# Kernel optimization log

Hardware: AMD Instinct MI355X
Metric: run time of the kernel (lower is better)

The kernel has to match this reference:

```python
import jax, jax.numpy as jnp
import numpy as np
import math

B, S, HID, H = 2, 2048, 1024, 16
D = HID // H  # head_dim = 64

def _get_slopes(n):
    # power-of-2 branch (n=16)
    start = 2 ** (-2 ** (-(math.log2(n) - 3)))
    return np.array([start * 2 ** (-i) for i in range(n)], dtype=np.float32)

def setup_inputs() -> dict:
    key = jax.random.key(0)
    ks = jax.random.split(key, 9)
    sc = 1.0 / math.sqrt(HID)
    return {
        "x":  jax.random.normal(ks[0], (B, S, HID), dtype=jnp.float32),
        "Wq": jax.random.normal(ks[1], (HID, HID), dtype=jnp.float32) * sc,
        "bq": jnp.zeros((HID,), dtype=jnp.float32),
        "Wk": jax.random.normal(ks[2], (HID, HID), dtype=jnp.float32) * sc,
        "bk": jnp.zeros((HID,), dtype=jnp.float32),
        "Wv": jax.random.normal(ks[3], (HID, HID), dtype=jnp.float32) * sc,
        "bv": jnp.zeros((HID,), dtype=jnp.float32),
        "Wo": jax.random.normal(ks[4], (HID, HID), dtype=jnp.float32) * sc,
        "bo": jnp.zeros((HID,), dtype=jnp.float32),
        "slopes": jnp.asarray(_get_slopes(H)),
    }

def reference(x, Wq, bq, Wk, bk, Wv, bv, Wo, bo, slopes):
    b, s, hid = x.shape
    h = slopes.shape[0]
    d = hid // h
    # projections (torch Linear: y = x @ W.T + b), split heads -> [b,h,s,d]
    q = (x @ Wq.T + bq).reshape(b, s, h, d).transpose(0, 2, 1, 3)
    k = (x @ Wk.T + bk).reshape(b, s, h, d).transpose(0, 2, 1, 3)
    v = (x @ Wv.T + bv).reshape(b, s, h, d).transpose(0, 2, 1, 3)
    scores = jnp.einsum('bhqd,bhkd->bhqk', q, k) / jnp.sqrt(jnp.float32(d))
    # ALiBi bias: slope_h * (j - i), shape [h,s,s]
    pos = jnp.arange(s)
    dist = (pos[None, :] - pos[:, None]).astype(x.dtype)  # [s,s]
    scores = scores + slopes[None, :, None, None] * dist[None, None]
    attn = jax.nn.softmax(scores, axis=-1)
    ctx = jnp.einsum('bhqk,bhkd->bhqd', attn, v)
    ctx = ctx.transpose(0, 2, 1, 3).reshape(b, s, hid)
    return ctx @ Wo.T + bo
```

## Files before the change

kernel.cpp:

```cpp
#include <hip/hip_runtime.h>
#include <stdint.h>

typedef __attribute__((ext_vector_type(8))) short bf16x8;
typedef __attribute__((ext_vector_type(4))) short bf16x4;
typedef __attribute__((ext_vector_type(4))) float f32x4;
typedef unsigned short u16t;

#define DEVINL static __device__ __forceinline__

DEVINL u16t f2bf(float f) {
  union { float f; unsigned u; } v; v.f = f;
  return (u16t)((v.u + 0x7FFFu + ((v.u >> 16) & 1u)) >> 16);
}
DEVINL float bf2f(u16t u) {
  union { unsigned u; float f; } v; v.u = ((unsigned)u) << 16; return v.f;
}

DEVINL float exp2_fast(float x) {
  float r; asm("v_exp_f32 %0, %1" : "=v"(r) : "v"(x)); return r;
}
DEVINL unsigned cvt_pk_bf16(float a, float b) {
  unsigned r; asm("v_cvt_pk_bf16_f32 %0, %1, %2" : "=v"(r) : "v"(a), "v"(b)); return r;
}
DEVINL float max3f(float a, float b, float c) {
  float r; asm("v_max3_f32 %0, %1, %2, %3" : "=v"(r) : "v"(a), "v"(b), "v"(c)); return r;
}

DEVINL void gload16(const void* g, void* l) {
  __builtin_amdgcn_global_load_lds((const __attribute__((address_space(1))) void*)g,
                                   (__attribute__((address_space(3))) void*)l, 16, 0, 0);
}

__global__ __launch_bounds__(256)
void cvt5_kernel(const float* __restrict__ x, const float* __restrict__ wq,
                 const float* __restrict__ wk, const float* __restrict__ wv,
                 const float* __restrict__ wo, u16t* __restrict__ x_bf,
                 u16t* __restrict__ wqkv, u16t* __restrict__ wo_bf) {
  const int bid = blockIdx.x;
  const float* src; u16t* dst; int off;
  if (bid < 2048) { src = x; dst = x_bf; off = bid * 2048; }
  else {
    const int j = bid - 2048, sel = j >> 9;
    off = (j & 511) * 2048;
    if (sel == 0)      { src = wq; dst = wqkv; }
    else if (sel == 1) { src = wk; dst = wqkv + 1048576; }
    else if (sel == 2) { src = wv; dst = wqkv + 2097152; }
    else               { src = wo; dst = wo_bf; }
  }
  const int i = off + threadIdx.x * 8;
  float4 a = *(const float4*)(src + i);
  float4 b = *(const float4*)(src + i + 4);
  union { bf16x8 v; u16t u[8]; } o;
  o.u[0] = f2bf(a.x); o.u[1] = f2bf(a.y); o.u[2] = f2bf(a.z); o.u[3] = f2bf(a.w);
  o.u[4] = f2bf(b.x); o.u[5] = f2bf(b.y); o.u[6] = f2bf(b.z); o.u[7] = f2bf(b.w);
  *(bf16x8*)(dst + i) = o.v;
}

template <int MODE>
__global__ __launch_bounds__(256, 3)
void gemm_kernel(const u16t* __restrict__ A, const u16t* __restrict__ Bw,
                 const float* __restrict__ bias0, const float* __restrict__ bias1,
                 const float* __restrict__ bias2, void* __restrict__ outp) {
  __shared__ __attribute__((aligned(16))) u16t As[128 * 64];
  __shared__ __attribute__((aligned(16))) u16t Bs[128 * 64];
  const int tid = threadIdx.x;
  const int w = tid >> 6, l = tid & 63;
  const int wm = w >> 1, wn = w & 1;
  const int bm = blockIdx.x, bn = blockIdx.y;
  const int g = l >> 4, r16 = l & 15;
  const int srow = l >> 3, sslot = l & 7;

  f32x4 acc[4][4];
#pragma unroll
  for (int m = 0; m < 4; ++m)
#pragma unroll
    for (int n = 0; n < 4; ++n) acc[m][n] = f32x4{0.f, 0.f, 0.f, 0.f};

  const size_t arow0 = (size_t)bm * 128;
  const size_t brow0 = (size_t)bn * 128;

  for (int kt = 0; kt < 16; ++kt) {
    __syncthreads();
#pragma unroll
    for (int i = 0; i < 4; ++i) {
      const int row = (i * 4 + w) * 8 + srow;
      const int colA = kt * 64 + ((sslot ^ (row & 7)) * 8);
      gload16(A + (arow0 + row) * 1024 + colA, (char*)As + (i * 4 + w) * 1024);
      gload16(Bw + (brow0 + row) * 1024 + colA, (char*)Bs + (i * 4 + w) * 1024);
    }
    asm volatile("s_waitcnt vmcnt(0)" ::: "memory");
    __syncthreads();
#pragma unroll
    for (int kk = 0; kk < 2; ++kk) {
      bf16x8 af[4], bfr[4];
#pragma unroll
      for (int m = 0; m < 4; ++m) {
        const int rr = wm * 64 + m * 16 + r16;
        af[m] = *(const bf16x8*)((const char*)As + rr * 128 + (((kk * 4 + g) ^ (rr & 7)) * 16));
      }
#pragma unroll
      for (int n = 0; n < 4; ++n) {
        const int rr = wn * 64 + n * 16 + r16;
        bfr[n] = *(const bf16x8*)((const char*)Bs + rr * 128 + (((kk * 4 + g) ^ (rr & 7)) * 16));
      }
#pragma unroll
      for (int m = 0; m < 4; ++m)
#pragma unroll
        for (int n = 0; n < 4; ++n)
          acc[m][n] = __builtin_amdgcn_mfma_f32_16x16x32_bf16(af[m], bfr[n], acc[m][n], 0, 0, 0);
    }
  }

  if (MODE == 0) {
    const int mat = bn >> 3;
    if (mat == 2) {
      u16t* vt = (u16t*)outp + 8388608u;
#pragma unroll
      for (int n = 0; n < 4; ++n) {
        const int col = ((bn & 7) * 128) + wn * 64 + n * 16 + r16;
        const int hh = col >> 6, dd = col & 63;
        const float bv = bias2[col];
#pragma unroll
        for (int m = 0; m < 4; ++m) {
          const int row0 = bm * 128 + wm * 64 + m * 16 + g * 4;
          const int b_ = row0 >> 11, s_ = row0 & 2047;
          union { bf16x4 v; u16t u[4]; } o4;
#pragma unroll
          for (int i = 0; i < 4; ++i) o4.u[i] = f2bf(acc[m][n][i] + bv);
          *(bf16x4*)(vt + ((size_t)(b_ * 16 + hh) * 64 + dd) * 2048 + s_) = o4.v;
        }
      }
    } else {
      const float* bias = (mat == 0) ? bias0 : bias1;
      const float scale = (mat == 0) ? 0.18033688f : 1.0f;
      u16t* o = (u16t*)outp + (size_t)mat * 4194304u;
#pragma unroll
      for (int n = 0; n < 4; ++n) {
        const int col = ((bn & 7) * 128) + wn * 64 + n * 16 + r16;
        const float bv = bias[col];
#pragma unroll
        for (int m = 0; m < 4; ++m) {
          const int row = bm * 128 + wm * 64 + m * 16 + g * 4;
#pragma unroll
          for (int i = 0; i < 4; ++i)
            o[(size_t)(row + i) * 1024 + col] = f2bf((acc[m][n][i] + bv) * scale);
        }
      }
    }
  } else {
    float* o = (float*)outp;
#pragma unroll
    for (int n = 0; n < 4; ++n) {
      const int col = bn * 128 + wn * 64 + n * 16 + r16;
      const float bv = bias0[col];
#pragma unroll
      for (int m = 0; m < 4; ++m) {
        const int row = bm * 128 + wm * 64 + m * 16 + g * 4;
#pragma unroll
        for (int i = 0; i < 4; ++i)
          o[(size_t)(row + i) * 1024 + col] = acc[m][n][i] + bv;
      }
    }
  }
}

__global__ __launch_bounds__(256, 2)
void attn_kernel(const u16t* __restrict__ Qb, const u16t* __restrict__ Kb,
                 const u16t* __restrict__ Vtb, const float* __restrict__ slopes,
                 u16t* __restrict__ O0, u16t* __restrict__ O1,
                 float2* __restrict__ ML) {
  __shared__ __attribute__((aligned(16))) u16t Kl[3][2048];
  __shared__ __attribute__((aligned(16))) u16t Vl[2][2048];
  const int tid = threadIdx.x;
  const int w = tid >> 6, l = tid & 63;
  const int g = l >> 4, r = l & 15;
  const int qt = blockIdx.x;
  const int slot = blockIdx.y >> 1, b = blockIdx.y & 1;
  int h, sp;
  if (slot < 10)       { h = 6 + slot;  sp = 1; }
  else if (slot < 19)  { h = slot - 3;  sp = 0; }
  else if (slot == 19) { h = 5; sp = 1; }
  else if (slot == 20) { h = 6; sp = 0; }
  else if (slot < 26)  { h = 25 - slot; sp = 1; }
  else                 { h = slot - 26; sp = 0; }
  const float slope2 = slopes[h] * 1.44269504f;
  const int qpos = qt * 64 + w * 16 + r;
  const size_t base = (size_t)b * 2097152 + (size_t)h * 64;

  const float Wkeys = 26.0f / slope2;
  const int wt = (int)ceilf(Wkeys * 0.03125f);
  const int n = sp ? (wt < 32 ? wt : 32)
                   : (wt - 32 < 0 ? 0 : (wt - 32 < 32 ? wt - 32 : 32));
  if (n == 0) {
    if (l < 16)
      ML[((size_t)(sp * 2 + b) * 16 + h) * 2048 + qpos] = float2{-3.0e38f, 0.f};
    return;
  }

  const u16t* qrow = Qb + base + (size_t)qpos * 1024;
  const bf16x8 qf0 = *(const bf16x8*)(qrow + g * 8);
  const bf16x8 qf1 = *(const bf16x8*)(qrow + 32 + g * 8);
  asm volatile("s_waitcnt vmcnt(0)" ::: "memory");

  const int sig = 8 * (r >> 2) + (r & 3);
  const int toffs[2] = {0, 4};
  int koff[2][2], voff[4];
#pragma unroll
  for (int t = 0; t < 2; ++t) {
    const int row = toffs[t] + sig;
    const int mk = (row & 3) ^ ((row >> 1) & 4);
#pragma unroll
    for (int hh = 0; hh < 2; ++hh) koff[t][hh] = row * 128 + (((hh * 4 + g) ^ mk) * 16);
  }
#pragma unroll
  for (int db = 0; db < 4; ++db)
    voff[db] = (8 * db + (r >> 1)) * 128 + ((((((r & 1) << 2) | g)) ^ ((r >> 1) & 3)) * 16);

  const int kline_s = w * 8 + (l >> 3);
  const int ku_s = ((l & 7) ^ ((kline_s & 3) ^ ((kline_s >> 1) & 4))) * 8;
  const int vu_s = (l & 7) ^ (kline_s & 3);
  const int vd_s = 2 * kline_s + (vu_s >> 2);
  const int vcol_s = (vu_s & 3) * 8;

  f32x4 cv[2];
#pragma unroll
  for (int t = 0; t < 2; ++t)
#pragma unroll
    for (int i = 0; i < 4; ++i) cv[t][i] = slope2 * (float)(toffs[t] + 8 * g + i);

  const float d32 = slope2 * 32.f;
  float mj = -3.0e38f;
  f32x4 oc[4], sacc;
#pragma unroll
  for (int d = 0; d < 4; ++d) oc[d] = f32x4{0.f, 0.f, 0.f, 0.f};
  sacc = f32x4{0.f, 0.f, 0.f, 0.f};
  union { bf16x8 v; u16t u[8]; } ones;
#pragma unroll
  for (int i = 0; i < 8; ++i) ones.u[i] = 0x3F80;

  const u16t* Krow = Kb + base;
  const u16t* Vrow = Vtb + (size_t)(b * 16 + h) * 131072;
  const int kt0 = sp * 32 + 31;

#define STAGE_K(kt_, b_)                                                          \
  gload16(Krow + (size_t)((kt_) * 32 + kline_s) * 1024 + ku_s,                    \
          (char*)Kl + (b_) * 4096 + w * 1024);
#define STAGE_V(kt_, b_)                                                          \
  gload16(Vrow + (size_t)vd_s * 2048 + (kt_) * 32 + vcol_s,                       \
          (char*)Vl + (b_) * 4096 + w * 1024);

  const int ktp = (n > 1) ? kt0 - 1 : kt0;
  STAGE_K(kt0, 0)
  STAGE_V(kt0, 0)
  STAGE_K(ktp, 1)

  for (int it = 0; it < n; ++it) {
    const int kt = kt0 - it;
    const int kbuf = it % 3, vbuf = it & 1;
    if (it == n - 1) { asm volatile("s_waitcnt vmcnt(0)" ::: "memory"); }
    else             { asm volatile("s_waitcnt vmcnt(1)" ::: "memory"); }
    __builtin_amdgcn_s_barrier();
    asm volatile("" ::: "memory");
    if (it + 1 < n) STAGE_V(kt - 1, vbuf ^ 1)
    if (it + 2 < n) STAGE_K(kt - 2, (it + 2) % 3)
    if (it) mj += d32;

    const char* KB = (const char*)Kl + kbuf * 4096;
    const char* VB = (const char*)Vl + vbuf * 4096;

    f32x4 st[2];
    __builtin_amdgcn_s_setprio(1);
#pragma unroll
    for (int t = 0; t < 2; ++t) {
      st[t] = __builtin_amdgcn_mfma_f32_16x16x32_bf16(
          *(const bf16x8*)(KB + koff[t][0]), qf0, cv[t], 0, 0, 0);
      st[t] = __builtin_amdgcn_mfma_f32_16x16x32_bf16(
          *(const bf16x8*)(KB + koff[t][1]), qf1, st[t], 0, 0, 0);
    }
    __builtin_amdgcn_s_setprio(0);

    const float m1 = max3f(st[0][0], st[0][1], st[0][2]);
    const float m2 = max3f(st[0][3], st[1][0], st[1][1]);
    const float m3 = max3f(st[1][2], st[1][3], m1);
    const float tm = fmaxf(m2, m3);
    if (__any(tm > mj)) {
      float tr = fmaxf(tm, __shfl_xor(tm, 16));
      tr = fmaxf(tr, __shfl_xor(tr, 32));
      const float mn = fmaxf(mj, tr);
      const float corr = exp2_fast(mj - mn);
#pragma unroll
      for (int d = 0; d < 4; ++d) {
        oc[d][0] *= corr; oc[d][1] *= corr; oc[d][2] *= corr; oc[d][3] *= corr;
      }
      sacc[0] *= corr; sacc[1] *= corr; sacc[2] *= corr; sacc[3] *= corr;
      mj = mn;
    }

    float pe[8];
#pragma unroll
    for (int t = 0; t < 2; ++t)
#pragma unroll
      for (int i = 0; i < 4; ++i) pe[t * 4 + i] = exp2_fast(st[t][i] - mj);
    union { bf16x8 v; unsigned q[4]; } pb;
#pragma unroll
    for (int j = 0; j < 4; ++j) pb.q[j] = cvt_pk_bf16(pe[j * 2], pe[j * 2 + 1]);

    __builtin_amdgcn_s_setprio(1);
#pragma unroll
    for (int db = 0; db < 4; ++db)
      oc[db] = __builtin_amdgcn_mfma_f32_16x16x32_bf16(
          *(const bf16x8*)(VB + voff[db]), pb.v, oc[db], 0, 0, 0);
    sacc = __builtin_amdgcn_mfma_f32_16x16x32_bf16(ones.v, pb.v, sacc, 0, 0, 0);
    __builtin_amdgcn_s_setprio(0);
  }
#undef STAGE_K
#undef STAGE_V

  u16t* op = (sp ? O1 : O0) + base + (size_t)qpos * 1024;
#pragma unroll
  for (int d = 0; d < 4; ++d) {
    union { bf16x4 v; u16t u[4]; } o4;
#pragma unroll
    for (int i = 0; i < 4; ++i) o4.u[i] = f2bf(oc[d][i]);
    *(bf16x4*)(op + d * 16 + g * 4) = o4.v;
  }
  if (l < 16) {
    const float m_global = mj + d32 * (float)(kt0 - n + 1);
    ML[((size_t)(sp * 2 + b) * 16 + h) * 2048 + qpos] = float2{m_global, sacc[0]};
  }
}

__global__ __launch_bounds__(256)
void combine_kernel(u16t* __restrict__ O0 ,
                    const u16t* __restrict__ O1, const float2* __restrict__ ML) {
  const int idx = blockIdx.x * 256 + threadIdx.x;
  const int colg = idx & 127, tok = idx >> 7;
  const int b = tok >> 11, s = tok & 2047, h = colg >> 3;
  const float2 ml0 = ML[((size_t)(0 + b) * 16 + h) * 2048 + s];
  const float2 ml1 = ML[((size_t)(2 + b) * 16 + h) * 2048 + s];
  const float M = fmaxf(ml0.x, ml1.x);
  const float e0 = exp2_fast(ml0.x - M), e1 = exp2_fast(ml1.x - M);
  const float invL = 1.f / (ml0.y * e0 + ml1.y * e1);
  const float w0 = e0 * invL, w1 = e1 * invL;
  union { bf16x8 v; u16t u[8]; } a, c, o;
  a.v = *(const bf16x8*)(O0 + (size_t)idx * 8);
  c.v = *(const bf16x8*)(O1 + (size_t)idx * 8);
#pragma unroll
  for (int i = 0; i < 8; ++i) o.u[i] = f2bf(bf2f(a.u[i]) * w0 + bf2f(c.u[i]) * w1);
  *(bf16x8*)(O0 + (size_t)idx * 8) = o.v;
}

extern "C" void kernel_launch(void* const* d_in, const int* in_sizes, int n_in,
                              void* d_out, int out_size, void* d_ws, size_t ws_size,
                              hipStream_t stream) {
  const float* x = (const float*)d_in[0];
  const float* Wq = (const float*)d_in[1];
  const float* bq = (const float*)d_in[2];
  const float* Wk = (const float*)d_in[3];
  const float* bk = (const float*)d_in[4];
  const float* Wv = (const float*)d_in[5];
  const float* bv = (const float*)d_in[6];
  const float* Wo = (const float*)d_in[7];
  const float* bo = (const float*)d_in[8];
  const float* slopes = (const float*)d_in[9];
  if (ws_size < (size_t)(48u << 20)) return;
  char* ws = (char*)d_ws;
  u16t* x_bf = (u16t*)(ws);
  u16t* wqkv = (u16t*)(ws + (8u << 20));
  u16t* wo_bf = (u16t*)(ws + (14u << 20));
  u16t* q_bf = (u16t*)(ws + (16u << 20));
  u16t* ctx_bf = (u16t*)(ws + (40u << 20));
  u16t* part1 = (u16t*)(ws);
  float2* ml = (float2*)(ws + (8u << 20));

  cvt5_kernel<<<4096, 256, 0, stream>>>(x, Wq, Wk, Wv, Wo, x_bf, wqkv, wo_bf);
  gemm_kernel<0><<<dim3(32, 24), 256, 0, stream>>>(x_bf, wqkv, bq, bk, bv, (void*)q_bf);
  attn_kernel<<<dim3(32, 64), 256, 0, stream>>>(q_bf, q_bf + 4194304, q_bf + 8388608,
                                                slopes, ctx_bf, part1, ml);
  combine_kernel<<<2048, 256, 0, stream>>>(ctx_bf, part1, ml);
  gemm_kernel<1><<<dim3(32, 8), 256, 0, stream>>>(ctx_bf, wo_bf, bo, bo, bo, d_out);
}
```

Baseline: 111.2 us.

## Use 512-thread attention blocks with split K/V loader waves and triple buffering

```diff
diff --git a/kernel.cpp b/kernel.cpp
--- a/kernel.cpp
+++ b/kernel.cpp
@@ -164,13 +164,13 @@
   }
 }
 
-__global__ __launch_bounds__(256, 2)
+__global__ __launch_bounds__(512, 4)
 void attn_kernel(const u16t* __restrict__ Qb, const u16t* __restrict__ Kb,
                  const u16t* __restrict__ Vtb, const float* __restrict__ slopes,
                  u16t* __restrict__ O0, u16t* __restrict__ O1,
                  float2* __restrict__ ML) {
   __shared__ __attribute__((aligned(16))) u16t Kl[3][2048];
-  __shared__ __attribute__((aligned(16))) u16t Vl[2][2048];
+  __shared__ __attribute__((aligned(16))) u16t Vl[3][2048];
   const int tid = threadIdx.x;
   const int w = tid >> 6, l = tid & 63;
   const int g = l >> 4, r = l & 15;
@@ -184,7 +184,7 @@
   else if (slot < 26)  { h = 25 - slot; sp = 1; }
   else                 { h = slot - 26; sp = 0; }
   const float slope2 = slopes[h] * 1.44269504f;
-  const int qpos = qt * 64 + w * 16 + r;
+  const int qpos = qt * 128 + w * 16 + r;
   const size_t base = (size_t)b * 2097152 + (size_t)h * 64;
 
   const float Wkeys = 26.0f / slope2;
@@ -216,11 +216,30 @@
   for (int db = 0; db < 4; ++db)
     voff[db] = (8 * db + (r >> 1)) * 128 + ((((((r & 1) << 2) | g)) ^ ((r >> 1) & 3)) * 16);
 
-  const int kline_s = w * 8 + (l >> 3);
-  const int ku_s = ((l & 7) ^ ((kline_s & 3) ^ ((kline_s >> 1) & 4))) * 8;
-  const int vu_s = (l & 7) ^ (kline_s & 3);
-  const int vd_s = 2 * kline_s + (vu_s >> 2);
-  const int vcol_s = (vu_s & 3) * 8;
+  const u16t* Krow = Kb + base;
+  const u16t* Vrow = Vtb + (size_t)(b * 16 + h) * 131072;
+  const int kt0 = sp * 32 + 31;
+
+  const int role = (w >= 4);
+  const int ts = tid & 255;
+  const int line = ts >> 3;
+  const char* gptr;
+  int gstep;
+  if (!role) {
+    const int ku = ((ts & 7) ^ ((line & 3) ^ ((line >> 1) & 4))) * 8;
+    gptr = (const char*)(Krow + (size_t)(kt0 * 32 + line) * 1024 + ku);
+    gstep = 32 * 1024 * 2;
+  } else {
+    const int vu = (ts & 7) ^ (line & 3);
+    const int vd = 2 * line + (vu >> 2);
+    const int vcol = (vu & 3) * 8;
+    gptr = (const char*)(Vrow + (size_t)vd * 2048 + kt0 * 32 + vcol);
+    gstep = 32 * 2;
+  }
+  char* lbase = role ? (char*)Vl : (char*)Kl;
+  const int loff = ts * 16;
+
+#define STAGE(BUF) { gload16(gptr, lbase + (BUF) * 4096 + loff); gptr -= gstep; }
 
   f32x4 cv[2];
 #pragma unroll
@@ -229,7 +248,7 @@
     for (int i = 0; i < 4; ++i) cv[t][i] = slope2 * (float)(toffs[t] + 8 * g + i);
 
   const float d32 = slope2 * 32.f;
-  float mj = -3.0e38f;
+  float mj = -3.0e38f - 0.f;
   f32x4 oc[4], sacc;
 #pragma unroll
   for (int d = 0; d < 4; ++d) oc[d] = f32x4{0.f, 0.f, 0.f, 0.f};
@@ -238,36 +257,7 @@
 #pragma unroll
   for (int i = 0; i < 8; ++i) ones.u[i] = 0x3F80;
 
-  const u16t* Krow = Kb + base;
-  const u16t* Vrow = Vtb + (size_t)(b * 16 + h) * 131072;
-  const int kt0 = sp * 32 + 31;
-
-#define STAGE_K(kt_, b_)                                                          \
-  gload16(Krow + (size_t)((kt_) * 32 + kline_s) * 1024 + ku_s,                    \
-          (char*)Kl + (b_) * 4096 + w * 1024);
-#define STAGE_V(kt_, b_)                                                          \
-  gload16(Vrow + (size_t)vd_s * 2048 + (kt_) * 32 + vcol_s,                       \
-          (char*)Vl + (b_) * 4096 + w * 1024);
-
-  const int ktp = (n > 1) ? kt0 - 1 : kt0;
-  STAGE_K(kt0, 0)
-  STAGE_V(kt0, 0)
-  STAGE_K(ktp, 1)
-
-  for (int it = 0; it < n; ++it) {
-    const int kt = kt0 - it;
-    const int kbuf = it % 3, vbuf = it & 1;
-    if (it == n - 1) { asm volatile("s_waitcnt vmcnt(0)" ::: "memory"); }
-    else             { asm volatile("s_waitcnt vmcnt(1)" ::: "memory"); }
-    __builtin_amdgcn_s_barrier();
-    asm volatile("" ::: "memory");
-    if (it + 1 < n) STAGE_V(kt - 1, vbuf ^ 1)
-    if (it + 2 < n) STAGE_K(kt - 2, (it + 2) % 3)
-    if (it) mj += d32;
-
-    const char* KB = (const char*)Kl + kbuf * 4096;
-    const char* VB = (const char*)Vl + vbuf * 4096;
-
+  auto compute_tile = [&](const char* KB, const char* VB) {
     f32x4 st[2];
     __builtin_amdgcn_s_setprio(1);
 #pragma unroll
@@ -278,6 +268,12 @@
           *(const bf16x8*)(KB + koff[t][1]), qf1, st[t], 0, 0, 0);
     }
     __builtin_amdgcn_s_setprio(0);
+
+    float pe[8];
+#pragma unroll
+    for (int t = 0; t < 2; ++t)
+#pragma unroll
+      for (int i = 0; i < 4; ++i) pe[t * 4 + i] = exp2_fast(st[t][i] - mj);
 
     const float m1 = max3f(st[0][0], st[0][1], st[0][2]);
     const float m2 = max3f(st[0][3], st[1][0], st[1][1]);
@@ -294,13 +290,12 @@
       }
       sacc[0] *= corr; sacc[1] *= corr; sacc[2] *= corr; sacc[3] *= corr;
       mj = mn;
-    }
-
-    float pe[8];
-#pragma unroll
-    for (int t = 0; t < 2; ++t)
-#pragma unroll
-      for (int i = 0; i < 4; ++i) pe[t * 4 + i] = exp2_fast(st[t][i] - mj);
+#pragma unroll
+      for (int t = 0; t < 2; ++t)
+#pragma unroll
+        for (int i = 0; i < 4; ++i) pe[t * 4 + i] = exp2_fast(st[t][i] - mj);
+    }
+
     union { bf16x8 v; unsigned q[4]; } pb;
 #pragma unroll
     for (int j = 0; j < 4; ++j) pb.q[j] = cvt_pk_bf16(pe[j * 2], pe[j * 2 + 1]);
@@ -312,9 +307,32 @@
           *(const bf16x8*)(VB + voff[db]), pb.v, oc[db], 0, 0, 0);
     sacc = __builtin_amdgcn_mfma_f32_16x16x32_bf16(ones.v, pb.v, sacc, 0, 0, 0);
     __builtin_amdgcn_s_setprio(0);
-  }
-#undef STAGE_K
-#undef STAGE_V
+  };
+
+#define ITER(IT, BUF)                                                             \
+  {                                                                               \
+    if ((IT) == n - 1) { asm volatile("s_waitcnt vmcnt(0)" ::: "memory"); }       \
+    else               { asm volatile("s_waitcnt vmcnt(1)" ::: "memory"); }       \
+    __builtin_amdgcn_s_barrier();                                                 \
+    asm volatile("" ::: "memory");                                                \
+    if ((IT) + 2 < n) STAGE((((BUF) + 2) % 3))                                    \
+    mj += d32;                                                                    \
+    compute_tile((const char*)Kl + (BUF) * 4096, (const char*)Vl + (BUF) * 4096); \
+  }
+
+  STAGE(0)
+  STAGE(1)
+
+  int it = 0;
+  for (; it + 3 <= n; it += 3) {
+    ITER(it, 0)
+    ITER(it + 1, 1)
+    ITER(it + 2, 2)
+  }
+  if (it < n)     ITER(it, 0)
+  if (it + 1 < n) ITER(it + 1, 1)
+#undef ITER
+#undef STAGE
 
   u16t* op = (sp ? O1 : O0) + base + (size_t)qpos * 1024;
 #pragma unroll
@@ -375,7 +393,7 @@
 
   cvt5_kernel<<<4096, 256, 0, stream>>>(x, Wq, Wk, Wv, Wo, x_bf, wqkv, wo_bf);
   gemm_kernel<0><<<dim3(32, 24), 256, 0, stream>>>(x_bf, wqkv, bq, bk, bv, (void*)q_bf);
-  attn_kernel<<<dim3(32, 64), 256, 0, stream>>>(q_bf, q_bf + 4194304, q_bf + 8388608,
+  attn_kernel<<<dim3(16, 64), 512, 0, stream>>>(q_bf, q_bf + 4194304, q_bf + 8388608,
                                                 slopes, ctx_bf, part1, ml);
   combine_kernel<<<2048, 256, 0, stream>>>(ctx_bf, part1, ml);
   gemm_kernel<1><<<dim3(32, 8), 256, 0, stream>>>(ctx_bf, wo_bf, bo, bo, bo, d_out);
```

Result: slower. 115.2 us (+3.6%).
